# Optimization experiments

Measured on AMD Instinct MI355X. Metric: run time of the kernel, lower is better.

## Reference

```python
import jax, jax.numpy as jnp
import numpy as np

DIM = 768
HEADS = 12
HEAD_DIM = DIM // HEADS
SCALE = HEAD_DIM ** (-0.5)


def setup_inputs() -> dict:
    key = jax.random.key(0)
    k1, k2, k3 = jax.random.split(key, 3)
    x = jax.random.normal(k1, (4, 2048, DIM), dtype=jnp.float32)
    # nn.Linear(dim, 3*dim, bias=False): weight [3*dim, dim]
    w_qkv = jax.random.normal(k2, (3 * DIM, DIM), dtype=jnp.float32) * (DIM ** -0.5)
    # nn.Linear(dim, dim) with bias
    w_proj = jax.random.normal(k3, (DIM, DIM), dtype=jnp.float32) * (DIM ** -0.5)
    b_proj = jnp.zeros((DIM,), dtype=jnp.float32)
    return {"x": x, "w_qkv": w_qkv, "w_proj": w_proj, "b_proj": b_proj}


def reference(x, w_qkv, w_proj, b_proj):
    B, N, C = x.shape
    H, D = HEADS, HEAD_DIM
    qkv = jnp.einsum('bnc,oc->bno', x, w_qkv)  # [B,N,3C]
    qkv = qkv.reshape(B, N, 3, H, D).transpose(2, 0, 3, 1, 4)  # [3,B,H,N,D]
    q, k, v = qkv[0], qkv[1], qkv[2]
    attn = jnp.einsum('bhnd,bhmd->bhnm', q, k) * SCALE  # [B,H,N,N]
    attn = jax.nn.softmax(attn, axis=-1)
    attn = jax.nn.softmax(attn, axis=-1)  # double softmax, as in original
    out = jnp.einsum('bhnm,bhmd->bhnd', attn, v)  # [B,H,N,D]
    out = out.transpose(0, 2, 1, 3).reshape(B, N, C)
    return jnp.einsum('bnc,oc->bno', out, w_proj) + b_proj
```

## Files before the change

### kernel.cpp

```cpp
#include <hip/hip_runtime.h>
#include <hip/hip_bf16.h>

#define DIM 768
#define HEADS 12
#define HD 64
#define SEQ 2048
#define BATCH 4
#define BHN 48
#define TOK 8192

#if __has_builtin(__builtin_amdgcn_exp2f)
#define EXP2F __builtin_amdgcn_exp2f
#else
#define EXP2F exp2f
#endif
#define EXP_C 0.1803368801111244f

using short8  = __attribute__((ext_vector_type(8))) short;
using short4v = __attribute__((ext_vector_type(4))) short;
using float4v = __attribute__((ext_vector_type(4))) float;

__device__ __forceinline__ short f2b(float f) {
    union { float f; unsigned u; } v; v.f = f;
    unsigned r = v.u + 0x7FFF + ((v.u >> 16) & 1);
    return (short)(r >> 16);
}
__device__ __forceinline__ float b2f(short s) {
    union { unsigned u; float f; } v;
    v.u = ((unsigned)(unsigned short)s) << 16;
    return v.f;
}
__device__ __forceinline__ unsigned pk2(float a, float b) {
    union { float f; unsigned u; } x, y; x.f = a; y.f = b;
    return __builtin_amdgcn_perm(x.u + 0x8000u, y.u + 0x8000u, 0x03020706u);
}

typedef const __attribute__((address_space(1))) unsigned GU;
typedef __attribute__((address_space(3))) unsigned LU;
__device__ __forceinline__ void gload_lds16(const short* g, short* l) {
    __builtin_amdgcn_global_load_lds((GU*)g, (LU*)l, 16, 0, 0);
}

__global__ void cast_all(const float* __restrict__ x, const float* __restrict__ wq,
                         const float* __restrict__ wp,
                         short* __restrict__ xb, short* __restrict__ wqb,
                         short* __restrict__ wpb, float* __restrict__ Vsum,
                         int nx4, int nq4) {
    int i = blockIdx.x * 256 + threadIdx.x;
    if (i < BHN * 64) Vsum[i] = 0.f;
    const float* in; short* out; int j = i;
    if (i < nx4)            { in = x;  out = xb;  }
    else if (i < nx4 + nq4) { in = wq; out = wqb; j = i - nx4; }
    else                    { in = wp; out = wpb; j = i - nx4 - nq4; }
    float4 f = ((const float4*)in)[j];
    short4 o;
    o.x = f2b(f.x); o.y = f2b(f.y); o.z = f2b(f.z); o.w = f2b(f.w);
    ((short4*)out)[j] = o;
}

__global__ __launch_bounds__(256, 3)
void gemm_qkv(const short* __restrict__ A, const short* __restrict__ Bw,
              short* __restrict__ Qw, short* __restrict__ Kw, short* __restrict__ Vw,
              float* __restrict__ Vsum)
{
    __shared__ __align__(16) short As[3][128 * 32];
    __shared__ __align__(16) short Bs[3][128 * 32];

    const int tid  = threadIdx.x;
    const int lane = tid & 63;
    const int wave = tid >> 6;
    const int wm = (wave >> 1) * 64, wn = (wave & 1) * 64;
    const int l15 = lane & 15, quad = lane >> 4;

    const int gid = blockIdx.x;
    const int w   = gid >> 3;
    const int ybl = (gid & 7) * 8 + (w & 7);
    const int xbl = w >> 3;

    const bool vpart = (xbl >= 12);
    const short* rowsP = vpart ? (Bw + 1536 * 768) : A;
    const short* colsP = vpart ? A : Bw;
    const int m0 = vpart ? (xbl - 12) * 128 : ybl * 128;
    const int n0 = vpart ? ybl * 128 : xbl * 128;
    const int K = DIM;

    float4v acc[4][4];
    #pragma unroll
    for (int i = 0; i < 4; i++)
        #pragma unroll
        for (int j = 0; j < 4; j++)
            acc[i][j] = (float4v){0.f, 0.f, 0.f, 0.f};

    const int G0 = wave * 128 + lane;
    const int G1 = G0 + 64;
    const int rA0 = G0 >> 2, cA0 = (G0 & 3) * 8;
    const int rA1 = G1 >> 2, cA1 = (G1 & 3) * 8;
    const int ldsoff = wave * 1024;

    auto STAGE = [&](int t, int buf) {
        const int kc = t * 32;
        gload_lds16(&rowsP[(size_t)(m0 + rA0) * K + kc + cA0], &As[buf][ldsoff]);
        gload_lds16(&rowsP[(size_t)(m0 + rA1) * K + kc + cA1], &As[buf][ldsoff + 512]);
        gload_lds16(&colsP[(size_t)(n0 + rA0) * K + kc + cA0], &Bs[buf][ldsoff]);
        gload_lds16(&colsP[(size_t)(n0 + rA1) * K + kc + cA1], &Bs[buf][ldsoff + 512]);
    };

    STAGE(0, 0);
    STAGE(1, 1);

    int cur = 0, nx2 = 2;
    for (int t = 0; t < 24; t++) {
        if (t < 23) { asm volatile("s_waitcnt vmcnt(4)" ::: "memory"); }
        else        { asm volatile("s_waitcnt vmcnt(0)" ::: "memory"); }
        __builtin_amdgcn_sched_barrier(0);
        __builtin_amdgcn_s_barrier();
        __builtin_amdgcn_sched_barrier(0);

        short8 af[4], bfr[4];
        #pragma unroll
        for (int tt = 0; tt < 4; tt++) {
            af[tt]  = *(const short8*)&As[cur][(wm + tt * 16 + l15) * 32 + quad * 8];
            bfr[tt] = *(const short8*)&Bs[cur][(wn + tt * 16 + l15) * 32 + quad * 8];
        }
        #pragma unroll
        for (int tm = 0; tm < 4; tm++)
            #pragma unroll
            for (int tn = 0; tn < 4; tn++)
                acc[tm][tn] = __builtin_amdgcn_mfma_f32_16x16x32_bf16(af[tm], bfr[tn], acc[tm][tn], 0, 0, 0);

        if (t < 22) STAGE(t + 2, nx2);
        cur = (cur == 2) ? 0 : cur + 1;
        nx2 = (nx2 == 2) ? 0 : nx2 + 1;
    }

    #pragma unroll
    for (int tm = 0; tm < 4; tm++)
        #pragma unroll
        for (int tn = 0; tn < 4; tn++)
            #pragma unroll
            for (int r = 0; r < 4; r++) {
                int row = m0 + wm + tm * 16 + quad * 4 + r;
                int col = n0 + wn + tn * 16 + l15;
                float v = acc[tm][tn][r];
                if (vpart) {
                    int hh = row >> 6, d = row & 63;
                    int b = col >> 11, n = col & 2047;
                    int bh = b * HEADS + hh;
                    int t2 = n >> 6, c2h = (n >> 5) & 1, wk = n & 31;
                    int slot = ((wk & 15) >> 2) * 8 + ((wk & 16) >> 2) + (wk & 3);
                    int g2 = c2h * 4 + (slot >> 3);
                    int gp2 = g2 ^ (d & 7);
                    Vw[(size_t)bh * (SEQ * 64) + t2 * 4096 + d * 64 + gp2 * 8 + (slot & 7)] = f2b(v);
                } else {
                    int hh = (col & 767) >> 6, d = col & 63;
                    int b = row >> 11, n = row & 2047;
                    int bh = b * HEADS + hh;
                    size_t idx = (size_t)bh * (SEQ * 64) + (size_t)n * 64
                               + (((d >> 3) ^ (n & 7)) << 3) + (d & 7);
                    if (col < 768) Qw[idx] = f2b(v * EXP_C);
                    else           Kw[idx] = f2b(v);
                }
            }

    if (vpart) {
        const int bb = n0 >> 11;
        #pragma unroll
        for (int tm = 0; tm < 4; tm++)
            #pragma unroll
            for (int r = 0; r < 4; r++) {
                float s4 = (acc[tm][0][r] + acc[tm][1][r]) + (acc[tm][2][r] + acc[tm][3][r]);
                #pragma unroll
                for (int m = 1; m < 16; m <<= 1) s4 += __shfl_xor(s4, m, 64);
                if (l15 == 0) {
                    int row = m0 + wm + tm * 16 + quad * 4 + r;
                    int hh = row >> 6, d = row & 63;
                    atomicAdd(&Vsum[(bb * HEADS + hh) * 64 + d], s4);
                }
            }
    }
}

__global__ __launch_bounds__(256, 4)
void gemm_proj(const short* __restrict__ A, const short* __restrict__ Bw,
               const float* __restrict__ bias, float* __restrict__ Out)
{
    __shared__ __align__(16) short As[3][128 * 32];
    __shared__ __align__(16) short Bs[3][64 * 32];

    const int tid  = threadIdx.x;
    const int lane = tid & 63;
    const int wave = tid >> 6;
    const int wm = (wave >> 1) * 64, wn = (wave & 1) * 32;
    const int l15 = lane & 15, quad = lane >> 4;

    const int gid = blockIdx.x;
    const int w   = gid >> 3;
    const int ybl = (gid & 7) * 8 + (w & 7);
    const int xbl = w >> 3;
    const int m0 = ybl * 128, n0 = xbl * 64;
    const int K = DIM;

    float4v acc[4][2];
    #pragma unroll
    for (int i = 0; i < 4; i++)
        #pragma unroll
        for (int j = 0; j < 2; j++)
            acc[i][j] = (float4v){0.f, 0.f, 0.f, 0.f};

    const int GA0 = wave * 128 + lane, GA1 = GA0 + 64;
    const int rA0 = GA0 >> 2, cA0 = (GA0 & 3) * 8;
    const int rA1 = GA1 >> 2, cA1 = (GA1 & 3) * 8;
    const int GB0 = wave * 64 + lane;
    const int rB0 = GB0 >> 2, cB0 = (GB0 & 3) * 8;
    const int ldsoffA = wave * 1024, ldsoffB = wave * 512;

    auto STAGE = [&](int t, int buf) {
        const int kc = t * 32;
        gload_lds16(&A [(size_t)(m0 + rA0) * K + kc + cA0], &As[buf][ldsoffA]);
        gload_lds16(&A [(size_t)(m0 + rA1) * K + kc + cA1], &As[buf][ldsoffA + 512]);
        gload_lds16(&Bw[(size_t)(n0 + rB0) * K + kc + cB0], &Bs[buf][ldsoffB]);
    };

    STAGE(0, 0);
    STAGE(1, 1);

    int cur = 0, nx2 = 2;
    for (int t = 0; t < 24; t++) {
        if (t < 23) { asm volatile("s_waitcnt vmcnt(3)" ::: "memory"); }
        else        { asm volatile("s_waitcnt vmcnt(0)" ::: "memory"); }
        __builtin_amdgcn_sched_barrier(0);
        __builtin_amdgcn_s_barrier();
        __builtin_amdgcn_sched_barrier(0);

        short8 af[4], bfr[2];
        #pragma unroll
        for (int tt = 0; tt < 4; tt++)
            af[tt] = *(const short8*)&As[cur][(wm + tt * 16 + l15) * 32 + quad * 8];
        #pragma unroll
        for (int tt = 0; tt < 2; tt++)
            bfr[tt] = *(const short8*)&Bs[cur][(wn + tt * 16 + l15) * 32 + quad * 8];
        #pragma unroll
        for (int tm = 0; tm < 4; tm++)
            #pragma unroll
            for (int tn = 0; tn < 2; tn++)
                acc[tm][tn] = __builtin_amdgcn_mfma_f32_16x16x32_bf16(af[tm], bfr[tn], acc[tm][tn], 0, 0, 0);

        if (t < 22) STAGE(t + 2, nx2);
        cur = (cur == 2) ? 0 : cur + 1;
        nx2 = (nx2 == 2) ? 0 : nx2 + 1;
    }

    #pragma unroll
    for (int tm = 0; tm < 4; tm++)
        #pragma unroll
        for (int tn = 0; tn < 2; tn++)
            #pragma unroll
            for (int r = 0; r < 4; r++) {
                int row = m0 + wm + tm * 16 + quad * 4 + r;
                int col = n0 + wn + tn * 16 + l15;
                Out[(size_t)row * 768 + col] = acc[tm][tn][r] + bias[col];
            }
}

__global__ __launch_bounds__(256, 3)
void attn_kernel(const short* __restrict__ Qw, const short* __restrict__ Kw,
                 const short* __restrict__ Vw, const float* __restrict__ Vsum,
                 short* __restrict__ Ow)
{
    __shared__ __align__(16) short LDS[24576];

    const int tid  = threadIdx.x;
    const int lane = tid & 63, wave = tid >> 6;
    const int l15 = lane & 15, quad = lane >> 4;
    const int r7  = l15 & 7;
    const int bid = blockIdx.x;
    const int ii  = bid >> 3;
    const int bh  = (bid & 7) * 6 + (ii >> 4);
    const int qt  = ii & 15;
    const int wq  = wave * 32;

    const short* Qp = Qw + (size_t)bh * (SEQ * 64) + qt * 8192;
    const short* Kp = Kw + (size_t)bh * (SEQ * 64);
    const short* Vp = Vw + (size_t)bh * (SEQ * 64);

    short8 onesf;
    #pragma unroll
    for (int j = 0; j < 8; j++) onesf[j] = (l15 == 0) ? (short)0x3F80 : (short)0;

    #pragma unroll
    for (int h = 0; h < 4; h++) {
        const int g = wave * 4 + h;
        gload_lds16(&Qp[g * 512 + lane * 8], &LDS[g * 512]);
    }
    __syncthreads();
    short8 aq[2][2];
    #pragma unroll
    for (int nb = 0; nb < 2; nb++)
        #pragma unroll
        for (int kk = 0; kk < 2; kk++) {
            int r = wq + nb * 16 + l15;
            aq[nb][kk] = *(const short8*)&LDS[r * 64 + (((kk * 4 + quad) ^ r7) << 3)];
        }
    __syncthreads();

    float4v Aacc[2][4], Lacc[2];
    #pragma unroll
    for (int mb = 0; mb < 2; mb++) {
        Lacc[mb] = (float4v){0.f, 0.f, 0.f, 0.f};
        #pragma unroll
        for (int t = 0; t < 4; t++) Aacc[mb][t] = (float4v){0.f, 0.f, 0.f, 0.f};
    }

    auto STAGE = [&](int t2, int kbuf) {
        const int kb = kbuf * 4096;
        #pragma unroll
        for (int h = 0; h < 2; h++) {
            const int g = wave * 2 + h;
            gload_lds16(&Kp[(size_t)t2 * 4096 + g * 512 + lane * 8], &LDS[kb + g * 512]);
            gload_lds16(&Vp[(size_t)t2 * 4096 + g * 512 + lane * 8], &LDS[12288 + kb + g * 512]);
        }
    };

    STAGE(0, 0);
    STAGE(1, 1);

    int cur = 0, nx2 = 2;
    for (int kt = 0; kt < 32; kt++) {
        if (kt < 31) { asm volatile("s_waitcnt vmcnt(4)" ::: "memory"); }
        else         { asm volatile("s_waitcnt vmcnt(0)" ::: "memory"); }
        __builtin_amdgcn_sched_barrier(0);
        __builtin_amdgcn_s_barrier();
        __builtin_amdgcn_sched_barrier(0);

        const short* KB = &LDS[cur * 4096];
        const short* VB = &LDS[12288 + cur * 4096];

        #pragma unroll
        for (int c2 = 0; c2 < 2; c2++) {
            union AE { unsigned u[4]; short8 s; };
            AE ae[2];
            #pragma unroll
            for (int tn2 = 0; tn2 < 2; tn2++) {
                const int row = (c2 * 2 + tn2) * 16 + l15;
                const short* rp = &KB[row * 64];
                short8 b0 = *(const short8*)&rp[(quad ^ r7) << 3];
                short8 b1 = *(const short8*)&rp[((4 + quad) ^ r7) << 3];
                #pragma unroll
                for (int nb = 0; nb < 2; nb++) {
                    float4v s = (float4v){0.f, 0.f, 0.f, 0.f};
                    s = __builtin_amdgcn_mfma_f32_16x16x32_bf16(b0, aq[nb][0], s, 0, 0, 0);
                    s = __builtin_amdgcn_mfma_f32_16x16x32_bf16(b1, aq[nb][1], s, 0, 0, 0);
                    ae[nb].u[tn2 * 2]     = pk2(EXP2F(s[0]), EXP2F(s[1]));
                    ae[nb].u[tn2 * 2 + 1] = pk2(EXP2F(s[2]), EXP2F(s[3]));
                }
            }
            __builtin_amdgcn_s_setprio(1);
            Lacc[0] = __builtin_amdgcn_mfma_f32_16x16x32_bf16(ae[0].s, onesf, Lacc[0], 0, 0, 0);
            Lacc[1] = __builtin_amdgcn_mfma_f32_16x16x32_bf16(ae[1].s, onesf, Lacc[1], 0, 0, 0);
            #pragma unroll
            for (int tn = 0; tn < 4; tn++) {
                const int d = tn * 16 + l15;
                short8 bv = *(const short8*)&VB[d * 64 + (((c2 * 4 + quad) ^ r7) << 3)];
                Aacc[0][tn] = __builtin_amdgcn_mfma_f32_16x16x32_bf16(ae[0].s, bv, Aacc[0][tn], 0, 0, 0);
                Aacc[1][tn] = __builtin_amdgcn_mfma_f32_16x16x32_bf16(ae[1].s, bv, Aacc[1][tn], 0, 0, 0);
            }
            __builtin_amdgcn_s_setprio(0);
        }

        if (kt < 30) STAGE(kt + 2, nx2);
        cur = (cur == 2) ? 0 : cur + 1;
        nx2 = (nx2 == 2) ? 0 : nx2 + 1;
    }

    const int b = bh / HEADS, hh = bh - (bh / HEADS) * HEADS;
    #pragma unroll
    for (int mb = 0; mb < 2; mb++)
        #pragma unroll
        for (int r = 0; r < 4; r++) {
            float il = 1.f / __shfl(Lacc[mb][r], lane & 48, 64);
            int row = qt * 128 + wq + mb * 16 + quad * 4 + r;
            int tok = b * SEQ + row;
            #pragma unroll
            for (int tn = 0; tn < 4; tn++) {
                int d = tn * 16 + l15;
                float vs = Vsum[bh * 64 + d];
                float val = (vs + Aacc[mb][tn][r] * il) * (1.f / 2049.f);
                Ow[(size_t)tok * 768 + hh * 64 + d] = f2b(val);
            }
        }
}

extern "C" void kernel_launch(void* const* d_in, const int* in_sizes, int n_in,
                              void* d_out, int out_size, void* d_ws, size_t ws_size,
                              hipStream_t stream) {
    const float* x      = (const float*)d_in[0];
    const float* w_qkv  = (const float*)d_in[1];
    const float* w_proj = (const float*)d_in[2];
    const float* b_proj = (const float*)d_in[3];
    float* out = (float*)d_out;

    char* ws = (char*)d_ws;
    size_t off = 0;
    auto alloc = [&](size_t bytes) {
        void* p = ws + off;
        off += (bytes + 255) & ~(size_t)255;
        return p;
    };
    short* x_bf  = (short*)alloc((size_t)TOK * DIM * 2);
    short* wq_bf = (short*)alloc((size_t)3 * DIM * DIM * 2);
    short* wp_bf = (short*)alloc((size_t)DIM * DIM * 2);
    short* Qw    = (short*)alloc((size_t)BHN * SEQ * 64 * 2);
    short* Kw    = (short*)alloc((size_t)BHN * SEQ * 64 * 2);
    short* Vw    = (short*)alloc((size_t)BHN * SEQ * 64 * 2);
    short* Ow    = (short*)alloc((size_t)TOK * DIM * 2);
    float* Vsum  = (float*)alloc((size_t)BHN * 64 * 4);

    int nx4 = TOK * DIM / 4, nq4 = 3 * DIM * DIM / 4, np4 = DIM * DIM / 4;
    int tot4 = nx4 + nq4 + np4;
    cast_all<<<tot4 / 256, 256, 0, stream>>>(x, w_qkv, w_proj, x_bf, wq_bf, wp_bf, Vsum, nx4, nq4);

    gemm_qkv<<<1152, 256, 0, stream>>>(x_bf, wq_bf, Qw, Kw, Vw, Vsum);

    attn_kernel<<<BHN * 16, 256, 0, stream>>>(Qw, Kw, Vw, Vsum, Ow);

    gemm_proj<<<768, 256, 0, stream>>>(Ow, wp_bf, b_proj, out);
}
```

Before: 198.5 us.

## Replace triple-buffered QKV GEMM pipeline with synchronous 64-wide K steps; stagger attention chunks

The QKV projection GEMM drops its three-stage async LDS pipeline and instead loads two 32-wide K slices per iteration, then syncs and computes. This cuts LDS use so the occupancy target can rise from 3 to 4 blocks. The cost is that load latency is no longer hidden behind compute within a block. In the attention kernel, odd waves now walk the two K chunks in reverse order, to spread out LDS bank and port contention.

Measured after the change: 201.5 us. About the same (+1.5%).

```diff
diff --git a/kernel.cpp b/kernel.cpp
--- a/kernel.cpp
+++ b/kernel.cpp
@@ -58,13 +58,13 @@
     ((short4*)out)[j] = o;
 }
 
-__global__ __launch_bounds__(256, 3)
+__global__ __launch_bounds__(256, 4)
 void gemm_qkv(const short* __restrict__ A, const short* __restrict__ Bw,
               short* __restrict__ Qw, short* __restrict__ Kw, short* __restrict__ Vw,
               float* __restrict__ Vsum)
 {
-    __shared__ __align__(16) short As[3][128 * 32];
-    __shared__ __align__(16) short Bs[3][128 * 32];
+    __shared__ __align__(16) short As[2][128 * 32];
+    __shared__ __align__(16) short Bs[2][128 * 32];
 
     const int tid  = threadIdx.x;
     const int lane = tid & 63;
@@ -97,40 +97,31 @@
     const int rA1 = G1 >> 2, cA1 = (G1 & 3) * 8;
     const int ldsoff = wave * 1024;
 
-    auto STAGE = [&](int t, int buf) {
-        const int kc = t * 32;
-        gload_lds16(&rowsP[(size_t)(m0 + rA0) * K + kc + cA0], &As[buf][ldsoff]);
-        gload_lds16(&rowsP[(size_t)(m0 + rA1) * K + kc + cA1], &As[buf][ldsoff + 512]);
-        gload_lds16(&colsP[(size_t)(n0 + rA0) * K + kc + cA0], &Bs[buf][ldsoff]);
-        gload_lds16(&colsP[(size_t)(n0 + rA1) * K + kc + cA1], &Bs[buf][ldsoff + 512]);
-    };
-
-    STAGE(0, 0);
-    STAGE(1, 1);
-
-    int cur = 0, nx2 = 2;
-    for (int t = 0; t < 24; t++) {
-        if (t < 23) { asm volatile("s_waitcnt vmcnt(4)" ::: "memory"); }
-        else        { asm volatile("s_waitcnt vmcnt(0)" ::: "memory"); }
-        __builtin_amdgcn_sched_barrier(0);
-        __builtin_amdgcn_s_barrier();
-        __builtin_amdgcn_sched_barrier(0);
-
-        short8 af[4], bfr[4];
-        #pragma unroll
-        for (int tt = 0; tt < 4; tt++) {
-            af[tt]  = *(const short8*)&As[cur][(wm + tt * 16 + l15) * 32 + quad * 8];
-            bfr[tt] = *(const short8*)&Bs[cur][(wn + tt * 16 + l15) * 32 + quad * 8];
-        }
-        #pragma unroll
-        for (int tm = 0; tm < 4; tm++)
-            #pragma unroll
-            for (int tn = 0; tn < 4; tn++)
-                acc[tm][tn] = __builtin_amdgcn_mfma_f32_16x16x32_bf16(af[tm], bfr[tn], acc[tm][tn], 0, 0, 0);
-
-        if (t < 22) STAGE(t + 2, nx2);
-        cur = (cur == 2) ? 0 : cur + 1;
-        nx2 = (nx2 == 2) ? 0 : nx2 + 1;
+    for (int kt = 0; kt < K; kt += 64) {
+        #pragma unroll
+        for (int s = 0; s < 2; s++) {
+            const int kc = kt + s * 32;
+            gload_lds16(&rowsP[(size_t)(m0 + rA0) * K + kc + cA0], &As[s][ldsoff]);
+            gload_lds16(&rowsP[(size_t)(m0 + rA1) * K + kc + cA1], &As[s][ldsoff + 512]);
+            gload_lds16(&colsP[(size_t)(n0 + rA0) * K + kc + cA0], &Bs[s][ldsoff]);
+            gload_lds16(&colsP[(size_t)(n0 + rA1) * K + kc + cA1], &Bs[s][ldsoff + 512]);
+        }
+        __syncthreads();
+        #pragma unroll
+        for (int s = 0; s < 2; s++) {
+            short8 af[4], bfr[4];
+            #pragma unroll
+            for (int t = 0; t < 4; t++) {
+                af[t]  = *(const short8*)&As[s][(wm + t * 16 + l15) * 32 + quad * 8];
+                bfr[t] = *(const short8*)&Bs[s][(wn + t * 16 + l15) * 32 + quad * 8];
+            }
+            #pragma unroll
+            for (int tm = 0; tm < 4; tm++)
+                #pragma unroll
+                for (int tn = 0; tn < 4; tn++)
+                    acc[tm][tn] = __builtin_amdgcn_mfma_f32_16x16x32_bf16(af[tm], bfr[tn], acc[tm][tn], 0, 0, 0);
+        }
+        __syncthreads();
     }
 
     #pragma unroll
@@ -324,6 +315,8 @@
     STAGE(0, 0);
     STAGE(1, 1);
 
+    const int wodd = wave & 1;
+
     int cur = 0, nx2 = 2;
     for (int kt = 0; kt < 32; kt++) {
         if (kt < 31) { asm volatile("s_waitcnt vmcnt(4)" ::: "memory"); }
@@ -336,7 +329,8 @@
         const short* VB = &LDS[12288 + cur * 4096];
 
         #pragma unroll
-        for (int c2 = 0; c2 < 2; c2++) {
+        for (int cc = 0; cc < 2; cc++) {
+            const int c2 = cc ^ wodd;
             union AE { unsigned u[4]; short8 s; };
             AE ae[2];
             #pragma unroll
```
